# Optimization experiments

Hardware: AMD Instinct MI355X
Metric: run time of the kernel (lower is better)

## Reference

```python
import jax, jax.numpy as jnp
import numpy as np

N_NODES = 50000
N_EDGES = 640000
N_REL = 200
D_IN = 128
D_OUT = 128


def setup_inputs() -> dict:
    key = jax.random.key(0)
    k1, k2, k3, k4, k5, k6 = jax.random.split(key, 6)
    x = jax.random.normal(k1, (N_NODES, D_IN), dtype=jnp.float32)
    edge_index = jax.random.randint(k2, (2, N_EDGES), 0, N_NODES, dtype=jnp.int64)
    edge_type = jax.random.randint(k3, (N_EDGES,), 0, N_REL, dtype=jnp.int64)
    rel_emb = jax.random.normal(k4, (N_REL, D_IN), dtype=jnp.float32)
    # nn.Linear weights stored as [out_features, in_features]
    W_lin = jax.random.normal(k5, (D_OUT, D_IN), dtype=jnp.float32) * (1.0 / np.sqrt(D_IN))
    # xavier_uniform for attn kernel [1, D_IN]
    limit = np.sqrt(6.0 / (1 + D_IN))
    W_attn = jax.random.uniform(k6, (1, D_IN), dtype=jnp.float32, minval=-limit, maxval=limit)
    return {"x": x, "edge_index": edge_index, "edge_type": edge_type,
            "rel_emb": rel_emb, "W_lin": W_lin, "W_attn": W_attn}


def reference(x, edge_index, edge_type, rel_emb, W_lin, W_attn):
    # x: [N, D_in]; edge_index: [2, E]; edge_type: [E]; rel_emb: [R, D_in]
    x_trans = x @ W_lin.T                       # [N, D_out]
    src_idx, tgt_idx = edge_index[0], edge_index[1]
    h_src = x[src_idx]                          # [E, D_in] gather
    h_rel = rel_emb[edge_type]                  # [E, D_in] gather
    sum_feat = h_src + h_rel                    # [E, D_in]
    attn = jax.nn.sigmoid(sum_feat @ W_attn.T)  # [E, 1]
    msg = x_trans[src_idx] * attn               # [E, D_out]
    out = jax.ops.segment_sum(msg, tgt_idx, num_segments=x.shape[0])  # [N, D_out]
    return jax.nn.relu(out)
```

## Files before the change

kernel.cpp:

```cpp
#include <hip/hip_runtime.h>
#include <hip/hip_bf16.h>

#define N_NODES 50000
#define N_EDGES 640000
#define N_REL   200
#define D       128
#define CAP     64
#define RANGES  8
#define NODES_PER_RANGE (N_NODES / RANGES)
#define CHUNK_EDGES 2560
#define N_CHUNKS (N_EDGES / CHUNK_EDGES)

#define XT_NG      3125
#define XT_WAVES2  (XT_NG * 2)
#define XT_BLOCKS  1563
#define SREL_BLOCKS 50
#define CNT_BLOCKS 196
#define PRE_BLOCKS (XT_BLOCKS + SREL_BLOCKS + CNT_BLOCKS)

#define G_BLOCKS_PER_RANGE 391

typedef __attribute__((ext_vector_type(8))) short short8;
typedef __attribute__((ext_vector_type(4))) float floatx4;
typedef __attribute__((ext_vector_type(4))) unsigned uintx4;

__device__ __forceinline__ unsigned short f2bf(float f) {
    unsigned u = __float_as_uint(f);
    u += 0x7FFF + ((u >> 16) & 1);
    return (unsigned short)(u >> 16);
}

__device__ __forceinline__ float sigmoidf(float x) {
    return 1.f / (1.f + __expf(-x));
}

__global__ __launch_bounds__(256) void pre_kernel(
        const float* __restrict__ x,
        const float* __restrict__ W,
        const float* __restrict__ rel,
        const float* __restrict__ Wattn,
        unsigned short* __restrict__ xt,
        float* __restrict__ s_node,
        float* __restrict__ s_rel,
        int* __restrict__ count) {
    __shared__ unsigned short lw[D * D];
    const int b = blockIdx.x;

    if (b < XT_BLOCKS) {
        const int tid = threadIdx.x;
#pragma unroll
        for (int i = 0; i < 8; ++i) {
            const int idx8 = tid + i * 256;
            const int row  = idx8 >> 4;
            const int kk   = idx8 & 15;
            const float* __restrict__ wr = W + (size_t)row * D + kk * 8;
            const float4 lo = *(const float4*)(wr);
            const float4 hi = *(const float4*)(wr + 4);
            short8 v;
            v[0] = (short)f2bf(lo.x); v[1] = (short)f2bf(lo.y);
            v[2] = (short)f2bf(lo.z); v[3] = (short)f2bf(lo.w);
            v[4] = (short)f2bf(hi.x); v[5] = (short)f2bf(hi.y);
            v[6] = (short)f2bf(hi.z); v[7] = (short)f2bf(hi.w);
            const int slot = (row * 16 + kk) ^ (row & 7);
            *(short8*)((char*)lw + slot * 16) = v;
        }
        __syncthreads();

        const int wv = b * 4 + (threadIdx.x >> 6);
        if (wv >= XT_WAVES2) return;
        const int ng   = wv >> 1;
        const int hf   = wv & 1;
        const int lane = threadIdx.x & 63;
        const int r16  = lane & 15;
        const int quad = lane >> 4;
        const int m0   = ng * 16;

        short8 af[4];
        float  sn = 0.f;
#pragma unroll
        for (int s = 0; s < 4; ++s) {
            const int k0 = s * 32 + quad * 8;
            const float* __restrict__ xr = x + (size_t)(m0 + r16) * D + k0;
            const float4 lo = *(const float4*)(xr);
            const float4 hi = *(const float4*)(xr + 4);
            if (hf == 0) {
                const float4 wl = *(const float4*)(Wattn + k0);
                const float4 wh = *(const float4*)(Wattn + k0 + 4);
                sn = fmaf(lo.x, wl.x, sn); sn = fmaf(lo.y, wl.y, sn);
                sn = fmaf(lo.z, wl.z, sn); sn = fmaf(lo.w, wl.w, sn);
                sn = fmaf(hi.x, wh.x, sn); sn = fmaf(hi.y, wh.y, sn);
                sn = fmaf(hi.z, wh.z, sn); sn = fmaf(hi.w, wh.w, sn);
            }
            short8 a;
            a[0] = (short)f2bf(lo.x); a[1] = (short)f2bf(lo.y);
            a[2] = (short)f2bf(lo.z); a[3] = (short)f2bf(lo.w);
            a[4] = (short)f2bf(hi.x); a[5] = (short)f2bf(hi.y);
            a[6] = (short)f2bf(hi.z); a[7] = (short)f2bf(hi.w);
            af[s] = a;
        }
        if (hf == 0) {
            sn += __shfl_xor(sn, 16);
            sn += __shfl_xor(sn, 32);
            if (lane < 16) s_node[m0 + r16] = sn;
        }

#pragma unroll
        for (int t = 0; t < 4; ++t) {
            const int tt = hf * 4 + t;
            floatx4 acc = {0.f, 0.f, 0.f, 0.f};
            const int row = tt * 16 + r16;
#pragma unroll
            for (int s = 0; s < 4; ++s) {
                const int slot = (row * 16 + s * 4 + quad) ^ (row & 7);
                const short8 bfrag = *(const short8*)((const char*)lw + slot * 16);
                acc = __builtin_amdgcn_mfma_f32_16x16x32_bf16(af[s], bfrag, acc, 0, 0, 0);
            }
#pragma unroll
            for (int r = 0; r < 4; ++r) {
                const int orow = m0 + quad * 4 + r;
                xt[(size_t)orow * D + tt * 16 + r16] = f2bf(acc[r]);
            }
        }
    } else if (b < XT_BLOCKS + SREL_BLOCKS) {
        const int wave = (b - XT_BLOCKS) * 4 + (threadIdx.x >> 6);
        const int lane = threadIdx.x & 63;
        if (wave < N_REL) {
            const float* __restrict__ row = rel + (size_t)wave * D;
            float a = fmaf(row[lane], Wattn[lane],
                           row[lane + 64] * Wattn[lane + 64]);
#pragma unroll
            for (int off = 32; off; off >>= 1)
                a += __shfl_down(a, off);
            if (lane == 0) s_rel[wave] = a;
        }
    } else {
        const int i = (b - XT_BLOCKS - SREL_BLOCKS) * 256 + threadIdx.x;
        if (i < N_NODES) count[i] = 0;
    }
}

__global__ __launch_bounds__(256) void scatter_kernel(
        const int* __restrict__ src_idx,
        const int* __restrict__ tgt_idx,
        const int* __restrict__ etype,
        const float* __restrict__ s_node,
        const float* __restrict__ s_rel,
        int* __restrict__ count,
        unsigned* __restrict__ sorted) {
    __shared__ float ls_rel[N_REL];
    if (threadIdx.x < N_REL) ls_rel[threadIdx.x] = s_rel[threadIdx.x];
    __syncthreads();

    const int b     = blockIdx.x;
    const int lo    = (b & 7) * NODES_PER_RANGE;
    const int hi    = lo + NODES_PER_RANGE;
    const int base  = (b >> 3) * CHUNK_EDGES + threadIdx.x;

#pragma unroll
    for (int it = 0; it < CHUNK_EDGES / 256; ++it) {
        const int e = base + it * 256;
        const int t = tgt_idx[e];
        const int s = src_idx[e];
        const int r = etype[e];
        if (t >= lo && t < hi) {
            const float logit = s_node[s] + ls_rel[r];
            const unsigned rec =
                ((unsigned)f2bf(sigmoidf(logit)) << 16) | (unsigned)s;
            const int k = atomicAdd(&count[t], 1);
            sorted[t * CAP + k] = rec;
        }
    }
}

__device__ __forceinline__ void gproc4(unsigned r, const unsigned short* __restrict__ xt,
                                       int sub, floatx4& a0, floatx4& a1) {
    const unsigned src = r & 0xFFFFu;
    const float a = __uint_as_float(r & 0xFFFF0000u);
    const uint4 p = *(const uint4*)(xt + (size_t)src * D + sub * 8);
    a0[0] = fmaf(a, __uint_as_float(p.x << 16),         a0[0]);
    a0[1] = fmaf(a, __uint_as_float(p.x & 0xFFFF0000u), a0[1]);
    a0[2] = fmaf(a, __uint_as_float(p.y << 16),         a0[2]);
    a0[3] = fmaf(a, __uint_as_float(p.y & 0xFFFF0000u), a0[3]);
    a1[0] = fmaf(a, __uint_as_float(p.z << 16),         a1[0]);
    a1[1] = fmaf(a, __uint_as_float(p.z & 0xFFFF0000u), a1[1]);
    a1[2] = fmaf(a, __uint_as_float(p.w << 16),         a1[2]);
    a1[3] = fmaf(a, __uint_as_float(p.w & 0xFFFF0000u), a1[3]);
}

__global__ __launch_bounds__(256) void gather_kernel(
        const int* __restrict__ count,
        const unsigned* __restrict__ sorted,
        const unsigned short* __restrict__ xt,
        float* __restrict__ out) {
    const int rng   = blockIdx.x & 7;
    const int idx   = blockIdx.x >> 3;
    const int w     = threadIdx.x >> 6;
    const int lane  = threadIdx.x & 63;
    const int q     = lane >> 4;
    const int sub   = lane & 15;
    const int local = idx * 16 + w * 4 + q;
    if (local >= NODES_PER_RANGE) return;
    const int t = rng * NODES_PER_RANGE + local;

    const int cnt = count[t];
    const unsigned* __restrict__ rec = sorted + (size_t)t * CAP;

    floatx4 a0 = {0.f, 0.f, 0.f, 0.f};
    floatx4 a1 = {0.f, 0.f, 0.f, 0.f};
    int i = 0;
    for (; i + 8 <= cnt; i += 8) {
        const uintx4 ra = __builtin_nontemporal_load((const uintx4*)(rec + i));
        const uintx4 rb = __builtin_nontemporal_load((const uintx4*)(rec + i + 4));
        gproc4(ra.x, xt, sub, a0, a1);
        gproc4(ra.y, xt, sub, a0, a1);
        gproc4(ra.z, xt, sub, a0, a1);
        gproc4(ra.w, xt, sub, a0, a1);
        gproc4(rb.x, xt, sub, a0, a1);
        gproc4(rb.y, xt, sub, a0, a1);
        gproc4(rb.z, xt, sub, a0, a1);
        gproc4(rb.w, xt, sub, a0, a1);
    }
    for (; i + 4 <= cnt; i += 4) {
        const uintx4 r4 = __builtin_nontemporal_load((const uintx4*)(rec + i));
        gproc4(r4.x, xt, sub, a0, a1);
        gproc4(r4.y, xt, sub, a0, a1);
        gproc4(r4.z, xt, sub, a0, a1);
        gproc4(r4.w, xt, sub, a0, a1);
    }
    for (; i < cnt; ++i)
        gproc4(__builtin_nontemporal_load(rec + i), xt, sub, a0, a1);

    floatx4 o0, o1;
    o0[0] = fmaxf(a0[0], 0.f); o0[1] = fmaxf(a0[1], 0.f);
    o0[2] = fmaxf(a0[2], 0.f); o0[3] = fmaxf(a0[3], 0.f);
    o1[0] = fmaxf(a1[0], 0.f); o1[1] = fmaxf(a1[1], 0.f);
    o1[2] = fmaxf(a1[2], 0.f); o1[3] = fmaxf(a1[3], 0.f);
    floatx4* orow = (floatx4*)(out + (size_t)t * D) + sub * 2;
    __builtin_nontemporal_store(o0, orow);
    __builtin_nontemporal_store(o1, orow + 1);
}

extern "C" void kernel_launch(void* const* d_in, const int* in_sizes, int n_in,
                              void* d_out, int out_size, void* d_ws, size_t ws_size,
                              hipStream_t stream) {
    const float* x        = (const float*)d_in[0];
    const int*   edge_idx = (const int*)d_in[1];
    const int*   etype    = (const int*)d_in[2];
    const float* rel_emb  = (const float*)d_in[3];
    const float* W_lin    = (const float*)d_in[4];
    const float* W_attn   = (const float*)d_in[5];
    float* out = (float*)d_out;

    const int* src_idx = edge_idx;
    const int* tgt_idx = edge_idx + N_EDGES;

    unsigned short* xt   = (unsigned short*)d_ws;
    float* s_node        = (float*)(xt + (size_t)N_NODES * D);
    float* s_rel         = s_node + N_NODES;
    int*   count         = (int*)(s_rel + N_REL);
    unsigned* sorted     = (unsigned*)(count + N_NODES);

    pre_kernel<<<dim3(PRE_BLOCKS), dim3(256), 0, stream>>>(
        x, W_lin, rel_emb, W_attn, xt, s_node, s_rel, count);

    scatter_kernel<<<dim3(N_CHUNKS * RANGES), dim3(256), 0, stream>>>(
        src_idx, tgt_idx, etype, s_node, s_rel, count, sorted);

    gather_kernel<<<dim3(G_BLOCKS_PER_RANGE * RANGES), dim3(256), 0, stream>>>(
        count, sorted, xt, out);
}
```

Baseline: 157.9 us.

## Fuse pre, scatter and gather into one cooperative persistent kernel

Replaces the three separate launches with a single cooperative kernel that runs the phases in grid-stride loops separated by grid-wide syncs. The bf16 conversion of W moves into a separate phase written to global memory, so the per-block LDS staging of W and its swizzle are dropped and MFMA B-fragments are read from global/L2. The aim is to remove kernel launch gaps and repeated per-block weight conversion. In exchange it adds three grid barriers, limits the grid to resident occupancy, and removes the 8-wide unroll in the gather loop.

```diff
diff --git a/kernel.cpp b/kernel.cpp
--- a/kernel.cpp
+++ b/kernel.cpp
@@ -1,5 +1,8 @@
 #include <hip/hip_runtime.h>
+#include <hip/hip_cooperative_groups.h>
 #include <hip/hip_bf16.h>
+
+namespace cg = cooperative_groups;
 
 #define N_NODES 50000
 #define N_EDGES 640000
@@ -11,14 +14,11 @@
 #define CHUNK_EDGES 2560
 #define N_CHUNKS (N_EDGES / CHUNK_EDGES)
 
-#define XT_NG      3125
-#define XT_WAVES2  (XT_NG * 2)
-#define XT_BLOCKS  1563
-#define SREL_BLOCKS 50
-#define CNT_BLOCKS 196
-#define PRE_BLOCKS (XT_BLOCKS + SREL_BLOCKS + CNT_BLOCKS)
-
-#define G_BLOCKS_PER_RANGE 391
+#define A0_UNITS 310
+#define A1_UNITS 1563
+#define XT_WAVES2 6250
+#define SC_UNITS (N_CHUNKS * RANGES)
+#define G_UNITS  (391 * RANGES)
 
 typedef __attribute__((ext_vector_type(8))) short short8;
 typedef __attribute__((ext_vector_type(4))) float floatx4;
@@ -32,144 +32,6 @@
 
 __device__ __forceinline__ float sigmoidf(float x) {
     return 1.f / (1.f + __expf(-x));
-}
-
-__global__ __launch_bounds__(256) void pre_kernel(
-        const float* __restrict__ x,
-        const float* __restrict__ W,
-        const float* __restrict__ rel,
-        const float* __restrict__ Wattn,
-        unsigned short* __restrict__ xt,
-        float* __restrict__ s_node,
-        float* __restrict__ s_rel,
-        int* __restrict__ count) {
-    __shared__ unsigned short lw[D * D];
-    const int b = blockIdx.x;
-
-    if (b < XT_BLOCKS) {
-        const int tid = threadIdx.x;
-#pragma unroll
-        for (int i = 0; i < 8; ++i) {
-            const int idx8 = tid + i * 256;
-            const int row  = idx8 >> 4;
-            const int kk   = idx8 & 15;
-            const float* __restrict__ wr = W + (size_t)row * D + kk * 8;
-            const float4 lo = *(const float4*)(wr);
-            const float4 hi = *(const float4*)(wr + 4);
-            short8 v;
-            v[0] = (short)f2bf(lo.x); v[1] = (short)f2bf(lo.y);
-            v[2] = (short)f2bf(lo.z); v[3] = (short)f2bf(lo.w);
-            v[4] = (short)f2bf(hi.x); v[5] = (short)f2bf(hi.y);
-            v[6] = (short)f2bf(hi.z); v[7] = (short)f2bf(hi.w);
-            const int slot = (row * 16 + kk) ^ (row & 7);
-            *(short8*)((char*)lw + slot * 16) = v;
-        }
-        __syncthreads();
-
-        const int wv = b * 4 + (threadIdx.x >> 6);
-        if (wv >= XT_WAVES2) return;
-        const int ng   = wv >> 1;
-        const int hf   = wv & 1;
-        const int lane = threadIdx.x & 63;
-        const int r16  = lane & 15;
-        const int quad = lane >> 4;
-        const int m0   = ng * 16;
-
-        short8 af[4];
-        float  sn = 0.f;
-#pragma unroll
-        for (int s = 0; s < 4; ++s) {
-            const int k0 = s * 32 + quad * 8;
-            const float* __restrict__ xr = x + (size_t)(m0 + r16) * D + k0;
-            const float4 lo = *(const float4*)(xr);
-            const float4 hi = *(const float4*)(xr + 4);
-            if (hf == 0) {
-                const float4 wl = *(const float4*)(Wattn + k0);
-                const float4 wh = *(const float4*)(Wattn + k0 + 4);
-                sn = fmaf(lo.x, wl.x, sn); sn = fmaf(lo.y, wl.y, sn);
-                sn = fmaf(lo.z, wl.z, sn); sn = fmaf(lo.w, wl.w, sn);
-                sn = fmaf(hi.x, wh.x, sn); sn = fmaf(hi.y, wh.y, sn);
-                sn = fmaf(hi.z, wh.z, sn); sn = fmaf(hi.w, wh.w, sn);
-            }
-            short8 a;
-            a[0] = (short)f2bf(lo.x); a[1] = (short)f2bf(lo.y);
-            a[2] = (short)f2bf(lo.z); a[3] = (short)f2bf(lo.w);
-            a[4] = (short)f2bf(hi.x); a[5] = (short)f2bf(hi.y);
-            a[6] = (short)f2bf(hi.z); a[7] = (short)f2bf(hi.w);
-            af[s] = a;
-        }
-        if (hf == 0) {
-            sn += __shfl_xor(sn, 16);
-            sn += __shfl_xor(sn, 32);
-            if (lane < 16) s_node[m0 + r16] = sn;
-        }
-
-#pragma unroll
-        for (int t = 0; t < 4; ++t) {
-            const int tt = hf * 4 + t;
-            floatx4 acc = {0.f, 0.f, 0.f, 0.f};
-            const int row = tt * 16 + r16;
-#pragma unroll
-            for (int s = 0; s < 4; ++s) {
-                const int slot = (row * 16 + s * 4 + quad) ^ (row & 7);
-                const short8 bfrag = *(const short8*)((const char*)lw + slot * 16);
-                acc = __builtin_amdgcn_mfma_f32_16x16x32_bf16(af[s], bfrag, acc, 0, 0, 0);
-            }
-#pragma unroll
-            for (int r = 0; r < 4; ++r) {
-                const int orow = m0 + quad * 4 + r;
-                xt[(size_t)orow * D + tt * 16 + r16] = f2bf(acc[r]);
-            }
-        }
-    } else if (b < XT_BLOCKS + SREL_BLOCKS) {
-        const int wave = (b - XT_BLOCKS) * 4 + (threadIdx.x >> 6);
-        const int lane = threadIdx.x & 63;
-        if (wave < N_REL) {
-            const float* __restrict__ row = rel + (size_t)wave * D;
-            float a = fmaf(row[lane], Wattn[lane],
-                           row[lane + 64] * Wattn[lane + 64]);
-#pragma unroll
-            for (int off = 32; off; off >>= 1)
-                a += __shfl_down(a, off);
-            if (lane == 0) s_rel[wave] = a;
-        }
-    } else {
-        const int i = (b - XT_BLOCKS - SREL_BLOCKS) * 256 + threadIdx.x;
-        if (i < N_NODES) count[i] = 0;
-    }
-}
-
-__global__ __launch_bounds__(256) void scatter_kernel(
-        const int* __restrict__ src_idx,
-        const int* __restrict__ tgt_idx,
-        const int* __restrict__ etype,
-        const float* __restrict__ s_node,
-        const float* __restrict__ s_rel,
-        int* __restrict__ count,
-        unsigned* __restrict__ sorted) {
-    __shared__ float ls_rel[N_REL];
-    if (threadIdx.x < N_REL) ls_rel[threadIdx.x] = s_rel[threadIdx.x];
-    __syncthreads();
-
-    const int b     = blockIdx.x;
-    const int lo    = (b & 7) * NODES_PER_RANGE;
-    const int hi    = lo + NODES_PER_RANGE;
-    const int base  = (b >> 3) * CHUNK_EDGES + threadIdx.x;
-
-#pragma unroll
-    for (int it = 0; it < CHUNK_EDGES / 256; ++it) {
-        const int e = base + it * 256;
-        const int t = tgt_idx[e];
-        const int s = src_idx[e];
-        const int r = etype[e];
-        if (t >= lo && t < hi) {
-            const float logit = s_node[s] + ls_rel[r];
-            const unsigned rec =
-                ((unsigned)f2bf(sigmoidf(logit)) << 16) | (unsigned)s;
-            const int k = atomicAdd(&count[t], 1);
-            sorted[t * CAP + k] = rec;
-        }
-    }
 }
 
 __device__ __forceinline__ void gproc4(unsigned r, const unsigned short* __restrict__ xt,
@@ -187,57 +49,172 @@
     a1[3] = fmaf(a, __uint_as_float(p.w & 0xFFFF0000u), a1[3]);
 }
 
-__global__ __launch_bounds__(256) void gather_kernel(
-        const int* __restrict__ count,
-        const unsigned* __restrict__ sorted,
-        const unsigned short* __restrict__ xt,
+__global__ void mono_kernel(
+        const float* __restrict__ x,
+        const float* __restrict__ W,
+        const float* __restrict__ rel,
+        const float* __restrict__ Wattn,
+        const int* __restrict__ src_idx,
+        const int* __restrict__ tgt_idx,
+        const int* __restrict__ etype,
+        unsigned short* __restrict__ Wbf,
+        unsigned short* __restrict__ xt,
+        float* __restrict__ s_node,
+        float* __restrict__ s_rel,
+        int* __restrict__ count,
+        unsigned* __restrict__ sorted,
         float* __restrict__ out) {
-    const int rng   = blockIdx.x & 7;
-    const int idx   = blockIdx.x >> 3;
-    const int w     = threadIdx.x >> 6;
-    const int lane  = threadIdx.x & 63;
-    const int q     = lane >> 4;
-    const int sub   = lane & 15;
-    const int local = idx * 16 + w * 4 + q;
-    if (local >= NODES_PER_RANGE) return;
-    const int t = rng * NODES_PER_RANGE + local;
-
-    const int cnt = count[t];
-    const unsigned* __restrict__ rec = sorted + (size_t)t * CAP;
-
-    floatx4 a0 = {0.f, 0.f, 0.f, 0.f};
-    floatx4 a1 = {0.f, 0.f, 0.f, 0.f};
-    int i = 0;
-    for (; i + 8 <= cnt; i += 8) {
-        const uintx4 ra = __builtin_nontemporal_load((const uintx4*)(rec + i));
-        const uintx4 rb = __builtin_nontemporal_load((const uintx4*)(rec + i + 4));
-        gproc4(ra.x, xt, sub, a0, a1);
-        gproc4(ra.y, xt, sub, a0, a1);
-        gproc4(ra.z, xt, sub, a0, a1);
-        gproc4(ra.w, xt, sub, a0, a1);
-        gproc4(rb.x, xt, sub, a0, a1);
-        gproc4(rb.y, xt, sub, a0, a1);
-        gproc4(rb.z, xt, sub, a0, a1);
-        gproc4(rb.w, xt, sub, a0, a1);
-    }
-    for (; i + 4 <= cnt; i += 4) {
-        const uintx4 r4 = __builtin_nontemporal_load((const uintx4*)(rec + i));
-        gproc4(r4.x, xt, sub, a0, a1);
-        gproc4(r4.y, xt, sub, a0, a1);
-        gproc4(r4.z, xt, sub, a0, a1);
-        gproc4(r4.w, xt, sub, a0, a1);
-    }
-    for (; i < cnt; ++i)
-        gproc4(__builtin_nontemporal_load(rec + i), xt, sub, a0, a1);
-
-    floatx4 o0, o1;
-    o0[0] = fmaxf(a0[0], 0.f); o0[1] = fmaxf(a0[1], 0.f);
-    o0[2] = fmaxf(a0[2], 0.f); o0[3] = fmaxf(a0[3], 0.f);
-    o1[0] = fmaxf(a1[0], 0.f); o1[1] = fmaxf(a1[1], 0.f);
-    o1[2] = fmaxf(a1[2], 0.f); o1[3] = fmaxf(a1[3], 0.f);
-    floatx4* orow = (floatx4*)(out + (size_t)t * D) + sub * 2;
-    __builtin_nontemporal_store(o0, orow);
-    __builtin_nontemporal_store(o1, orow + 1);
+    __shared__ float ls_rel[N_REL];
+    const int bid  = blockIdx.x;
+    const int tid  = threadIdx.x;
+    const int gdim = gridDim.x;
+    cg::grid_group gg = cg::this_grid();
+
+    for (int u = bid; u < A0_UNITS; u += gdim) {
+        if (u < 64) {
+            const int i = u * 256 + tid;
+            Wbf[i] = f2bf(W[i]);
+        } else if (u < 114) {
+            const int wave = (u - 64) * 4 + (tid >> 6);
+            const int lane = tid & 63;
+            if (wave < N_REL) {
+                const float* __restrict__ row = rel + (size_t)wave * D;
+                float a = fmaf(row[lane], Wattn[lane],
+                               row[lane + 64] * Wattn[lane + 64]);
+#pragma unroll
+                for (int off = 32; off; off >>= 1)
+                    a += __shfl_down(a, off);
+                if (lane == 0) s_rel[wave] = a;
+            }
+        } else {
+            const int i = (u - 114) * 256 + tid;
+            if (i < N_NODES) count[i] = 0;
+        }
+    }
+    __threadfence();
+    gg.sync();
+
+    for (int u = bid; u < A1_UNITS; u += gdim) {
+        const int wv = u * 4 + (tid >> 6);
+        if (wv < XT_WAVES2) {
+            const int ng   = wv >> 1;
+            const int hf   = wv & 1;
+            const int lane = tid & 63;
+            const int r16  = lane & 15;
+            const int quad = lane >> 4;
+            const int m0   = ng * 16;
+
+            short8 af[4];
+            float  sn = 0.f;
+#pragma unroll
+            for (int s = 0; s < 4; ++s) {
+                const int k0 = s * 32 + quad * 8;
+                const float* __restrict__ xr = x + (size_t)(m0 + r16) * D + k0;
+                const float4 lo = *(const float4*)(xr);
+                const float4 hi = *(const float4*)(xr + 4);
+                if (hf == 0) {
+                    const float4 wl = *(const float4*)(Wattn + k0);
+                    const float4 wh = *(const float4*)(Wattn + k0 + 4);
+                    sn = fmaf(lo.x, wl.x, sn); sn = fmaf(lo.y, wl.y, sn);
+                    sn = fmaf(lo.z, wl.z, sn); sn = fmaf(lo.w, wl.w, sn);
+                    sn = fmaf(hi.x, wh.x, sn); sn = fmaf(hi.y, wh.y, sn);
+                    sn = fmaf(hi.z, wh.z, sn); sn = fmaf(hi.w, wh.w, sn);
+                }
+                short8 a;
+                a[0] = (short)f2bf(lo.x); a[1] = (short)f2bf(lo.y);
+                a[2] = (short)f2bf(lo.z); a[3] = (short)f2bf(lo.w);
+                a[4] = (short)f2bf(hi.x); a[5] = (short)f2bf(hi.y);
+                a[6] = (short)f2bf(hi.z); a[7] = (short)f2bf(hi.w);
+                af[s] = a;
+            }
+            if (hf == 0) {
+                sn += __shfl_xor(sn, 16);
+                sn += __shfl_xor(sn, 32);
+                if (lane < 16) s_node[m0 + r16] = sn;
+            }
+
+#pragma unroll
+            for (int t = 0; t < 4; ++t) {
+                const int tt = hf * 4 + t;
+                floatx4 acc = {0.f, 0.f, 0.f, 0.f};
+#pragma unroll
+                for (int s = 0; s < 4; ++s) {
+                    const int k0 = s * 32 + quad * 8;
+                    const short8 bfrag =
+                        *(const short8*)(Wbf + (size_t)(tt * 16 + r16) * D + k0);
+                    acc = __builtin_amdgcn_mfma_f32_16x16x32_bf16(af[s], bfrag, acc, 0, 0, 0);
+                }
+#pragma unroll
+                for (int r = 0; r < 4; ++r) {
+                    const int orow = m0 + quad * 4 + r;
+                    xt[(size_t)orow * D + tt * 16 + r16] = f2bf(acc[r]);
+                }
+            }
+        }
+    }
+    __threadfence();
+    gg.sync();
+
+    if (tid < N_REL) ls_rel[tid] = s_rel[tid];
+    __syncthreads();
+    for (int u = bid; u < SC_UNITS; u += gdim) {
+        const int lo   = (u & 7) * NODES_PER_RANGE;
+        const int hi   = lo + NODES_PER_RANGE;
+        const int base = (u >> 3) * CHUNK_EDGES + tid;
+#pragma unroll
+        for (int it = 0; it < CHUNK_EDGES / 256; ++it) {
+            const int e = base + it * 256;
+            const int t = tgt_idx[e];
+            const int s = src_idx[e];
+            const int r = etype[e];
+            if (t >= lo && t < hi) {
+                const float logit = s_node[s] + ls_rel[r];
+                const unsigned rec =
+                    ((unsigned)f2bf(sigmoidf(logit)) << 16) | (unsigned)s;
+                const int k = atomicAdd(&count[t], 1);
+                sorted[t * CAP + k] = rec;
+            }
+        }
+    }
+    __threadfence();
+    gg.sync();
+
+    for (int u = bid; u < G_UNITS; u += gdim) {
+        const int rng   = u & 7;
+        const int idx   = u >> 3;
+        const int w     = tid >> 6;
+        const int lane  = tid & 63;
+        const int q     = lane >> 4;
+        const int sub   = lane & 15;
+        const int local = idx * 16 + w * 4 + q;
+        if (local < NODES_PER_RANGE) {
+            const int t = rng * NODES_PER_RANGE + local;
+            const int cnt = count[t];
+            const unsigned* __restrict__ rec = sorted + (size_t)t * CAP;
+
+            floatx4 a0 = {0.f, 0.f, 0.f, 0.f};
+            floatx4 a1 = {0.f, 0.f, 0.f, 0.f};
+            int i = 0;
+            for (; i + 4 <= cnt; i += 4) {
+                const uintx4 r4 = __builtin_nontemporal_load((const uintx4*)(rec + i));
+                gproc4(r4.x, xt, sub, a0, a1);
+                gproc4(r4.y, xt, sub, a0, a1);
+                gproc4(r4.z, xt, sub, a0, a1);
+                gproc4(r4.w, xt, sub, a0, a1);
+            }
+            for (; i < cnt; ++i)
+                gproc4(__builtin_nontemporal_load(rec + i), xt, sub, a0, a1);
+
+            floatx4 o0, o1;
+            o0[0] = fmaxf(a0[0], 0.f); o0[1] = fmaxf(a0[1], 0.f);
+            o0[2] = fmaxf(a0[2], 0.f); o0[3] = fmaxf(a0[3], 0.f);
+            o1[0] = fmaxf(a1[0], 0.f); o1[1] = fmaxf(a1[1], 0.f);
+            o1[2] = fmaxf(a1[2], 0.f); o1[3] = fmaxf(a1[3], 0.f);
+            floatx4* orow = (floatx4*)(out + (size_t)t * D) + sub * 2;
+            __builtin_nontemporal_store(o0, orow);
+            __builtin_nontemporal_store(o1, orow + 1);
+        }
+    }
 }
 
 extern "C" void kernel_launch(void* const* d_in, const int* in_sizes, int n_in,
@@ -257,15 +234,32 @@
     unsigned short* xt   = (unsigned short*)d_ws;
     float* s_node        = (float*)(xt + (size_t)N_NODES * D);
     float* s_rel         = s_node + N_NODES;
-    int*   count         = (int*)(s_rel + N_REL);
+    unsigned short* Wbf  = (unsigned short*)(s_rel + N_REL);
+    int*   count         = (int*)(Wbf + D * D);
     unsigned* sorted     = (unsigned*)(count + N_NODES);
 
-    pre_kernel<<<dim3(PRE_BLOCKS), dim3(256), 0, stream>>>(
-        x, W_lin, rel_emb, W_attn, xt, s_node, s_rel, count);
-
-    scatter_kernel<<<dim3(N_CHUNKS * RANGES), dim3(256), 0, stream>>>(
-        src_idx, tgt_idx, etype, s_node, s_rel, count, sorted);
-
-    gather_kernel<<<dim3(G_BLOCKS_PER_RANGE * RANGES), dim3(256), 0, stream>>>(
-        count, sorted, xt, out);
-}
+    static int grid = 0;
+    if (grid == 0) {
+        int dev = 0;
+        hipGetDevice(&dev);
+        hipDeviceProp_t prop;
+        hipGetDeviceProperties(&prop, dev);
+        int maxb = 0;
+        hipOccupancyMaxActiveBlocksPerMultiprocessor(&maxb, mono_kernel, 256, 0);
+        if (maxb < 1) maxb = 1;
+        long g = (long)maxb * prop.multiProcessorCount;
+        g &= ~7L;
+        if (g > 2048) g = 2048;
+        if (g < 8) g = 8;
+        grid = (int)g;
+    }
+
+    void* kargs[] = {
+        (void*)&x, (void*)&W_lin, (void*)&rel_emb, (void*)&W_attn,
+        (void*)&src_idx, (void*)&tgt_idx, (void*)&etype,
+        (void*)&Wbf, (void*)&xt, (void*)&s_node, (void*)&s_rel,
+        (void*)&count, (void*)&sorted, (void*)&out
+    };
+    hipLaunchCooperativeKernel((void*)mono_kernel,
+                               dim3(grid), dim3(256), kargs, 0, stream);
+}
```

New measurement: 501.3 us. 217% more time.
